# Performance work log

Hardware: AMD Instinct MI355X
Metric: run time of the kernel (lower is better)

The kernel has to match this reference:

```python
import jax, jax.numpy as jnp
import numpy as np

N = 8192
IN_DIM = 256
OUT_DIM = 256
NEG_INF = -1000000000.0
LEAKY_SLOPE = 0.2


def setup_inputs() -> dict:
    key = jax.random.key(0)
    k_h, k_adj, k_W, k_a = jax.random.split(key, 4)
    h = jax.random.normal(k_h, (N, IN_DIM), dtype=jnp.float32)
    adj = jax.random.randint(k_adj, (N, N), 0, 2, dtype=jnp.int32)
    # learned params (nn.Linear without bias stores weight [out, in]; we keep [in, out] for x @ W)
    W = jax.random.normal(k_W, (IN_DIM, OUT_DIM), dtype=jnp.float32) / np.sqrt(IN_DIM)
    a = jax.random.normal(k_a, (OUT_DIM,), dtype=jnp.float32) / np.sqrt(OUT_DIM)
    return {"h": h, "adj": adj, "W": W, "a": a}


def reference(h, adj, W, a):
    Wh = h @ W                                   # [N, out_dim]
    f = Wh @ a                                   # [N]
    e = jax.nn.leaky_relu(f[:, None] + f[None, :], LEAKY_SLOPE)  # [N, N]
    mask = (adj > 0).astype(Wh.dtype)
    e_masked = e * mask + (1.0 - mask) * NEG_INF
    alpha = jax.nn.softmax(e_masked, axis=1)     # [N, N]
    h_prime = alpha @ Wh                         # [N, out_dim]
    return jax.nn.elu(h_prime), alpha
```

## Files before the change

kernel.cpp:

```cpp
#include <hip/hip_runtime.h>
#include <hip/hip_bf16.h>

#define NROW 8192
#define DIM 256

typedef short bf16x8 __attribute__((ext_vector_type(8)));
typedef float f32x4 __attribute__((ext_vector_type(4)));

__device__ __forceinline__ short f2bf(float x) {
    return __builtin_bit_cast(short, __float2bfloat16(x));
}

__device__ __forceinline__ void gload_lds16(const void* g, void* l) {
    __builtin_amdgcn_global_load_lds(
        (const __attribute__((address_space(1))) unsigned int*)g,
        (__attribute__((address_space(3))) unsigned int*)l, 16, 0, 0);
}

__global__ __launch_bounds__(256) void k1_whgemm(
    const float* __restrict__ h, const float* __restrict__ W,
    const float* __restrict__ a, short* __restrict__ whbT,
    float* __restrict__ f)
{
    __shared__ float hs[64][65];
    __shared__ float wsm[64][65];
    const int tid = threadIdx.x;
    const int tx = tid & 15, ty = tid >> 4;
    const int i0 = blockIdx.x * 64;
    const int n0 = blockIdx.y * 64;

    float acc[4][4];
#pragma unroll
    for (int u = 0; u < 4; ++u)
#pragma unroll
        for (int v = 0; v < 4; ++v) acc[u][v] = 0.f;

    for (int kb = 0; kb < DIM; kb += 64) {
#pragma unroll
        for (int rr = 0; rr < 4; ++rr) {
            int row = rr * 16 + ty;
            *(float4*)&hs[row][tx * 4] =
                *(const float4*)&h[(size_t)(i0 + row) * DIM + kb + tx * 4];
            *(float4*)&wsm[row][tx * 4] =
                *(const float4*)&W[(size_t)(kb + row) * DIM + n0 + tx * 4];
        }
        __syncthreads();
#pragma unroll 8
        for (int kk = 0; kk < 64; ++kk) {
            float av[4], bv[4];
#pragma unroll
            for (int u = 0; u < 4; ++u) av[u] = hs[ty * 4 + u][kk];
#pragma unroll
            for (int v = 0; v < 4; ++v) bv[v] = wsm[kk][tx * 4 + v];
#pragma unroll
            for (int u = 0; u < 4; ++u)
#pragma unroll
                for (int v = 0; v < 4; ++v) acc[u][v] += av[u] * bv[v];
        }
        __syncthreads();
    }

#pragma unroll
    for (int u = 0; u < 4; ++u)
#pragma unroll
        for (int v = 0; v < 4; ++v) hs[ty * 4 + u][tx * 4 + v] = acc[u][v];
    __syncthreads();

    {
        int r = tid >> 2, q = tid & 3;
        float s = 0.f;
#pragma unroll
        for (int c = 0; c < 16; ++c) s += hs[r][q * 16 + c] * a[n0 + q * 16 + c];
        s += __shfl_xor(s, 1);
        s += __shfl_xor(s, 2);
        if (q == 0) atomicAdd(&f[i0 + r], s);
    }

    {
        int n = tid >> 2, q = tid & 3;
        union { short s[16]; int4 i4[2]; } pk;
#pragma unroll
        for (int b = 0; b < 4; ++b)
#pragma unroll
            for (int c = 0; c < 4; ++c)
                pk.s[b * 4 + c] = f2bf(hs[q * 16 + b * 4 + c][n]);
        size_t base = ((size_t)(i0 >> 6) * 256 + n0 + n) * 64 + q * 16;
        *(int4*)&whbT[base] = pk.i4[0];
        *(int4*)&whbT[base + 8] = pk.i4[1];
    }
}

__global__ __launch_bounds__(256) void k3d_alpha(
    const int* __restrict__ adj, const float* __restrict__ f,
    float* __restrict__ alpha)
{
    const int i = blockIdx.x;
    const int tid = threadIdx.x;
    const float fi = f[i];
    const int* row = adj + (size_t)i * NROW;

    int4 av[8];
    float4 fv[8];
#pragma unroll
    for (int it = 0; it < 8; ++it)
        av[it] = *(const int4*)&row[it * 1024 + tid * 4];
#pragma unroll
    for (int it = 0; it < 8; ++it)
        fv[it] = *(const float4*)&f[it * 1024 + tid * 4];

    float sum = 0.f;
#pragma unroll
    for (int it = 0; it < 8; ++it) {
        float x0 = fi + fv[it].x, x1 = fi + fv[it].y;
        float x2 = fi + fv[it].z, x3 = fi + fv[it].w;
        float4 t;
        t.x = av[it].x > 0 ? __expf(fmaxf(x0, 0.2f * x0)) : 0.f;
        t.y = av[it].y > 0 ? __expf(fmaxf(x1, 0.2f * x1)) : 0.f;
        t.z = av[it].z > 0 ? __expf(fmaxf(x2, 0.2f * x2)) : 0.f;
        t.w = av[it].w > 0 ? __expf(fmaxf(x3, 0.2f * x3)) : 0.f;
        fv[it] = t;
        sum += t.x + t.y + t.z + t.w;
    }

#pragma unroll
    for (int off = 32; off > 0; off >>= 1) sum += __shfl_xor(sum, off);
    __shared__ float red[4];
    if ((tid & 63) == 0) red[tid >> 6] = sum;
    __syncthreads();
    const float inv = 1.f / (red[0] + red[1] + red[2] + red[3]);

    float* arow = alpha + (size_t)i * NROW;
#pragma unroll
    for (int it = 0; it < 8; ++it) {
        float4 t = fv[it];
        float4 o = {t.x * inv, t.y * inv, t.z * inv, t.w * inv};
        *(float4*)&arow[it * 1024 + tid * 4] = o;
    }
}

__global__ __launch_bounds__(512) void k4g_gemm(
    const float* __restrict__ alpha, const short* __restrict__ whbT,
    float* __restrict__ out0)
{
    __shared__ __align__(16) short Bs[4][4096];

    const int tid = threadIdx.x;
    const int wave = tid >> 6;
    const int lane = tid & 63;
    const int lo = lane & 15;
    const int quad = lane >> 4;
    const int q8 = quad * 8;

    const int bid = blockIdx.x;
    const int xcd = bid & 7;
    const int slot = bid >> 3;
    const int rb = xcd * 8 + (slot & 7);
    const int cs = slot >> 3;
    const int i0 = rb * 128;
    const int n0 = cs * 64;

    const float* aptr = alpha + (size_t)(i0 + wave * 16 + lo) * NROW + q8;

    const int n_local = tid >> 3;
    const int schunk = ((tid & 7) ^ (n_local & 7)) * 8;

    const int bx0 = (quad ^ (lo & 7)) * 8;
    const int bx1 = ((4 + quad) ^ (lo & 7)) * 8;
    int off0[4], off1[4];
#pragma unroll
    for (int nt = 0; nt < 4; ++nt) {
        int rbase = (nt * 16 + lo) * 64;
        off0[nt] = rbase + bx0;
        off1[nt] = rbase + bx1;
    }

    f32x4 acc[4] = {};
    f32x4 aA[4], aB[4], aC[4], aD[4];

#define STAGE(buf, kt)                                                        \
    {                                                                         \
        const short* gsrc = whbT + (size_t)(kt) * 16384 +                     \
                            (n0 + n_local) * 64 + schunk;                     \
        gload_lds16(gsrc, &Bs[buf][tid * 8]);                                 \
    }

#define ALOAD(set, kt)                                                        \
    {                                                                         \
        const float* ap = aptr + (size_t)(kt) * 64;                           \
        asm volatile("global_load_dwordx4 %0, %4, off\n\t"                    \
                     "global_load_dwordx4 %1, %4, off offset:16\n\t"          \
                     "global_load_dwordx4 %2, %4, off offset:128\n\t"         \
                     "global_load_dwordx4 %3, %4, off offset:144"             \
                     : "=&v"(aA[set]), "=&v"(aB[set]),                        \
                       "=&v"(aC[set]), "=&v"(aD[set])                         \
                     : "v"(ap));                                              \
    }

#define CONSUME(c)                                                            \
    {                                                                         \
        bf16x8 af0, af1;                                                      \
        af0[0] = f2bf(aA[c][0]); af0[1] = f2bf(aA[c][1]);                     \
        af0[2] = f2bf(aA[c][2]); af0[3] = f2bf(aA[c][3]);                     \
        af0[4] = f2bf(aB[c][0]); af0[5] = f2bf(aB[c][1]);                     \
        af0[6] = f2bf(aB[c][2]); af0[7] = f2bf(aB[c][3]);                     \
        af1[0] = f2bf(aC[c][0]); af1[1] = f2bf(aC[c][1]);                     \
        af1[2] = f2bf(aC[c][2]); af1[3] = f2bf(aC[c][3]);                     \
        af1[4] = f2bf(aD[c][0]); af1[5] = f2bf(aD[c][1]);                     \
        af1[6] = f2bf(aD[c][2]); af1[7] = f2bf(aD[c][3]);                     \
        _Pragma("unroll")                                                     \
        for (int nt = 0; nt < 4; ++nt) {                                      \
            bf16x8 b0 = *(const bf16x8*)&Bs[c][off0[nt]];                     \
            acc[nt] = __builtin_amdgcn_mfma_f32_16x16x32_bf16(af0, b0,        \
                                                          acc[nt], 0, 0, 0);  \
            bf16x8 b1 = *(const bf16x8*)&Bs[c][off1[nt]];                     \
            acc[nt] = __builtin_amdgcn_mfma_f32_16x16x32_bf16(af1, b1,        \
                                                          acc[nt], 0, 0, 0);  \
        }                                                                     \
    }

#define KSTEP(kt, c, DO, N)                                                   \
    {                                                                         \
        if (DO) { STAGE(((c) + 2) & 3, (kt) + 2); ALOAD(((c) + 2) & 3,        \
                                                        (kt) + 2); }          \
        asm volatile("s_waitcnt vmcnt(" #N ")" ::: "memory");                 \
        __builtin_amdgcn_s_barrier();                                         \
        __builtin_amdgcn_sched_barrier(0);                                    \
        CONSUME(c)                                                            \
    }

    STAGE(0, 0); ALOAD(0, 0);
    STAGE(1, 1); ALOAD(1, 1);

#pragma unroll 1
    for (int base = 0; base < 124; base += 4) {
        KSTEP(base + 0, 0, true, 10)
        KSTEP(base + 1, 1, true, 10)
        KSTEP(base + 2, 2, true, 10)
        KSTEP(base + 3, 3, true, 10)
    }
    KSTEP(124, 0, true, 10)
    KSTEP(125, 1, true, 10)
    KSTEP(126, 2, false, 5)
    KSTEP(127, 3, false, 0)

#undef STAGE
#undef ALOAD
#undef CONSUME
#undef KSTEP

    const int ccb = n0 + lo;
#pragma unroll
    for (int nt = 0; nt < 4; ++nt) {
#pragma unroll
        for (int c = 0; c < 4; ++c) {
            const int rr = i0 + wave * 16 + quad * 4 + c;
            float v = acc[nt][c];
            v = v > 0.f ? v : __expf(v) - 1.f;
            out0[(size_t)rr * DIM + ccb + nt * 16] = v;
        }
    }
}

extern "C" void kernel_launch(void* const* d_in, const int* in_sizes, int n_in,
                              void* d_out, int out_size, void* d_ws, size_t ws_size,
                              hipStream_t stream) {
    const float* h = (const float*)d_in[0];
    const int* adj = (const int*)d_in[1];
    const float* W = (const float*)d_in[2];
    const float* a = (const float*)d_in[3];
    float* out0 = (float*)d_out;
    float* alpha = out0 + (size_t)NROW * DIM;

    char* ws = (char*)d_ws;
    float* f = (float*)ws;
    short* whbT = (short*)(ws + 32768);

    hipMemsetAsync(f, 0, NROW * sizeof(float), stream);
    k1_whgemm<<<dim3(NROW / 64, DIM / 64), 256, 0, stream>>>(h, W, a, whbT, f);
    k3d_alpha<<<dim3(NROW), 256, 0, stream>>>(adj, f, alpha);
    k4g_gemm<<<dim3(256), 512, 0, stream>>>(alpha, whbT, out0);
}
```

Baseline: 607.7 us.

## Fuse softmax alpha computation into the alpha@Wh GEMM kernel

Merges the separate alpha kernel into the GEMM kernel. Each GEMM block first streams its 128 rows of adj to compute the softmax row sums, then recomputes the exp values from adj on the fly during the MFMA loop. Each of the 4 column-slice blocks writes a quarter of alpha to the output. This removes the GEMM's reread of the fp32 alpha matrix and one launch, at the cost of reading adj twice per column slice (8 times in total) and redundant exp work across the 4 column blocks.

```diff
diff --git a/kernel.cpp b/kernel.cpp
--- a/kernel.cpp
+++ b/kernel.cpp
@@ -15,6 +15,28 @@
     __builtin_amdgcn_global_load_lds(
         (const __attribute__((address_space(1))) unsigned int*)g,
         (__attribute__((address_space(3))) unsigned int*)l, 16, 0, 0);
+}
+
+__device__ __forceinline__ float lrexpi(int m, float fj, float fi) {
+    float x = fi + fj;
+    return m > 0 ? __expf(fmaxf(x, 0.2f * x)) : 0.f;
+}
+__device__ __forceinline__ float sum4i(int4 m, float4 fv, float fi) {
+    return lrexpi(m.x, fv.x, fi) + lrexpi(m.y, fv.y, fi) +
+           lrexpi(m.z, fv.z, fi) + lrexpi(m.w, fv.w, fi);
+}
+__device__ __forceinline__ float lrexpb(float bits, float fj, float fi) {
+    int m = __builtin_bit_cast(int, bits);
+    float x = fi + fj;
+    return m > 0 ? __expf(fmaxf(x, 0.2f * x)) : 0.f;
+}
+__device__ __forceinline__ float4 lrexp4(f32x4 a, float4 fv, float fi) {
+    float4 r;
+    r.x = lrexpb(a[0], fv.x, fi);
+    r.y = lrexpb(a[1], fv.y, fi);
+    r.z = lrexpb(a[2], fv.z, fi);
+    r.w = lrexpb(a[3], fv.w, fi);
+    return r;
 }
 
 __global__ __launch_bounds__(256) void k1_whgemm(
@@ -90,58 +112,12 @@
     }
 }
 
-__global__ __launch_bounds__(256) void k3d_alpha(
+__global__ __launch_bounds__(512) void k45_fused(
     const int* __restrict__ adj, const float* __restrict__ f,
-    float* __restrict__ alpha)
-{
-    const int i = blockIdx.x;
-    const int tid = threadIdx.x;
-    const float fi = f[i];
-    const int* row = adj + (size_t)i * NROW;
-
-    int4 av[8];
-    float4 fv[8];
-#pragma unroll
-    for (int it = 0; it < 8; ++it)
-        av[it] = *(const int4*)&row[it * 1024 + tid * 4];
-#pragma unroll
-    for (int it = 0; it < 8; ++it)
-        fv[it] = *(const float4*)&f[it * 1024 + tid * 4];
-
-    float sum = 0.f;
-#pragma unroll
-    for (int it = 0; it < 8; ++it) {
-        float x0 = fi + fv[it].x, x1 = fi + fv[it].y;
-        float x2 = fi + fv[it].z, x3 = fi + fv[it].w;
-        float4 t;
-        t.x = av[it].x > 0 ? __expf(fmaxf(x0, 0.2f * x0)) : 0.f;
-        t.y = av[it].y > 0 ? __expf(fmaxf(x1, 0.2f * x1)) : 0.f;
-        t.z = av[it].z > 0 ? __expf(fmaxf(x2, 0.2f * x2)) : 0.f;
-        t.w = av[it].w > 0 ? __expf(fmaxf(x3, 0.2f * x3)) : 0.f;
-        fv[it] = t;
-        sum += t.x + t.y + t.z + t.w;
-    }
-
-#pragma unroll
-    for (int off = 32; off > 0; off >>= 1) sum += __shfl_xor(sum, off);
-    __shared__ float red[4];
-    if ((tid & 63) == 0) red[tid >> 6] = sum;
-    __syncthreads();
-    const float inv = 1.f / (red[0] + red[1] + red[2] + red[3]);
-
-    float* arow = alpha + (size_t)i * NROW;
-#pragma unroll
-    for (int it = 0; it < 8; ++it) {
-        float4 t = fv[it];
-        float4 o = {t.x * inv, t.y * inv, t.z * inv, t.w * inv};
-        *(float4*)&arow[it * 1024 + tid * 4] = o;
-    }
-}
-
-__global__ __launch_bounds__(512) void k4g_gemm(
-    const float* __restrict__ alpha, const short* __restrict__ whbT,
+    const short* __restrict__ whbT, float* __restrict__ alpha,
     float* __restrict__ out0)
 {
+    __shared__ float f_sh[NROW];
     __shared__ __align__(16) short Bs[4][4096];
 
     const int tid = threadIdx.x;
@@ -159,11 +135,59 @@
     const int i0 = rb * 128;
     const int n0 = cs * 64;
 
-    const float* aptr = alpha + (size_t)(i0 + wave * 16 + lo) * NROW + q8;
+#pragma unroll
+    for (int u = 0; u < 4; ++u)
+        *(float4*)&f_sh[u * 2048 + tid * 4] =
+            *(const float4*)&f[u * 2048 + tid * 4];
+    __syncthreads();
+
+    const int myrow = i0 + wave * 16 + lo;
+    const float fi = f_sh[myrow];
+    const int* adji = adj + (size_t)myrow * NROW + q8;
+
+    float rsum = 0.f;
+    {
+        int4 A0, A1, A2, A3, B0, B1, B2, B3;
+        int4 C0, C1, C2, C3, D0, D1, D2, D3;
+
+#define LOADI(P, kt)                                                          \
+        {                                                                     \
+            const int* p = adji + (size_t)(kt) * 64;                          \
+            P##0 = *(const int4*)p;                                           \
+            P##1 = *(const int4*)(p + 4);                                     \
+            P##2 = *(const int4*)(p + 32);                                    \
+            P##3 = *(const int4*)(p + 36);                                    \
+        }
+
+#define SUMI(P, kt)                                                           \
+        {                                                                     \
+            float4 F0 = *(const float4*)&f_sh[(kt) * 64 + q8];                \
+            float4 F1 = *(const float4*)&f_sh[(kt) * 64 + q8 + 4];            \
+            float4 F2 = *(const float4*)&f_sh[(kt) * 64 + 32 + q8];           \
+            float4 F3 = *(const float4*)&f_sh[(kt) * 64 + 36 + q8];           \
+            rsum += sum4i(P##0, F0, fi) + sum4i(P##1, F1, fi) +               \
+                    sum4i(P##2, F2, fi) + sum4i(P##3, F3, fi);                \
+        }
+
+        LOADI(A, 0) LOADI(B, 1) LOADI(C, 2) LOADI(D, 3)
+#pragma unroll 1
+        for (int kt = 0; kt < 124; kt += 4) {
+            SUMI(A, kt)     LOADI(A, kt + 4)
+            SUMI(B, kt + 1) LOADI(B, kt + 5)
+            SUMI(C, kt + 2) LOADI(C, kt + 6)
+            SUMI(D, kt + 3) LOADI(D, kt + 7)
+        }
+        SUMI(A, 124) SUMI(B, 125) SUMI(C, 126) SUMI(D, 127)
+#undef LOADI
+#undef SUMI
+    }
+
+    rsum += __shfl_xor(rsum, 16);
+    rsum += __shfl_xor(rsum, 32);
+    const float inv = 1.f / rsum;
 
     const int n_local = tid >> 3;
     const int schunk = ((tid & 7) ^ (n_local & 7)) * 8;
-
     const int bx0 = (quad ^ (lo & 7)) * 8;
     const int bx1 = ((4 + quad) ^ (lo & 7)) * 8;
     int off0[4], off1[4];
@@ -174,8 +198,10 @@
         off1[nt] = rbase + bx1;
     }
 
+    const float* adjp = (const float*)adji;
+
+    f32x4 pA[4], pB[4], pC[4], pD[4];
     f32x4 acc[4] = {};
-    f32x4 aA[4], aB[4], aC[4], aD[4];
 
 #define STAGE(buf, kt)                                                        \
     {                                                                         \
@@ -186,27 +212,50 @@
 
 #define ALOAD(set, kt)                                                        \
     {                                                                         \
-        const float* ap = aptr + (size_t)(kt) * 64;                           \
+        const float* ap = adjp + (size_t)(kt) * 64;                           \
         asm volatile("global_load_dwordx4 %0, %4, off\n\t"                    \
                      "global_load_dwordx4 %1, %4, off offset:16\n\t"          \
                      "global_load_dwordx4 %2, %4, off offset:128\n\t"         \
                      "global_load_dwordx4 %3, %4, off offset:144"             \
-                     : "=&v"(aA[set]), "=&v"(aB[set]),                        \
-                       "=&v"(aC[set]), "=&v"(aD[set])                         \
+                     : "=&v"(pA[set]), "=&v"(pB[set]),                        \
+                       "=&v"(pC[set]), "=&v"(pD[set])                         \
                      : "v"(ap));                                              \
     }
 
-#define CONSUME(c)                                                            \
+#define CONSUME(c, kt)                                                        \
     {                                                                         \
+        float4 F0 = *(const float4*)&f_sh[(kt) * 64 + q8];                    \
+        float4 F1 = *(const float4*)&f_sh[(kt) * 64 + q8 + 4];                \
+        float4 F2 = *(const float4*)&f_sh[(kt) * 64 + 32 + q8];               \
+        float4 F3 = *(const float4*)&f_sh[(kt) * 64 + 36 + q8];               \
+        float4 t0 = lrexp4(pA[c], F0, fi);                                    \
+        float4 t1 = lrexp4(pB[c], F1, fi);                                    \
+        float4 t2 = lrexp4(pC[c], F2, fi);                                    \
+        float4 t3 = lrexp4(pD[c], F3, fi);                                    \
+        float4 s0 = make_float4(t0.x * inv, t0.y * inv, t0.z * inv,           \
+                                t0.w * inv);                                  \
+        float4 s1 = make_float4(t1.x * inv, t1.y * inv, t1.z * inv,           \
+                                t1.w * inv);                                  \
+        float4 s2 = make_float4(t2.x * inv, t2.y * inv, t2.z * inv,           \
+                                t2.w * inv);                                  \
+        float4 s3 = make_float4(t3.x * inv, t3.y * inv, t3.z * inv,           \
+                                t3.w * inv);                                  \
+        if (((kt) & 3) == cs) {                                               \
+            float* arow = alpha + (size_t)myrow * NROW + (kt) * 64 + q8;      \
+            *(float4*)arow = s0;                                              \
+            *(float4*)(arow + 4) = s1;                                        \
+            *(float4*)(arow + 32) = s2;                                       \
+            *(float4*)(arow + 36) = s3;                                       \
+        }                                                                     \
         bf16x8 af0, af1;                                                      \
-        af0[0] = f2bf(aA[c][0]); af0[1] = f2bf(aA[c][1]);                     \
-        af0[2] = f2bf(aA[c][2]); af0[3] = f2bf(aA[c][3]);                     \
-        af0[4] = f2bf(aB[c][0]); af0[5] = f2bf(aB[c][1]);                     \
-        af0[6] = f2bf(aB[c][2]); af0[7] = f2bf(aB[c][3]);                     \
-        af1[0] = f2bf(aC[c][0]); af1[1] = f2bf(aC[c][1]);                     \
-        af1[2] = f2bf(aC[c][2]); af1[3] = f2bf(aC[c][3]);                     \
-        af1[4] = f2bf(aD[c][0]); af1[5] = f2bf(aD[c][1]);                     \
-        af1[6] = f2bf(aD[c][2]); af1[7] = f2bf(aD[c][3]);                     \
+        af0[0] = f2bf(s0.x); af0[1] = f2bf(s0.y);                             \
+        af0[2] = f2bf(s0.z); af0[3] = f2bf(s0.w);                             \
+        af0[4] = f2bf(s1.x); af0[5] = f2bf(s1.y);                             \
+        af0[6] = f2bf(s1.z); af0[7] = f2bf(s1.w);                             \
+        af1[0] = f2bf(s2.x); af1[1] = f2bf(s2.y);                             \
+        af1[2] = f2bf(s2.z); af1[3] = f2bf(s2.w);                             \
+        af1[4] = f2bf(s3.x); af1[5] = f2bf(s3.y);                             \
+        af1[6] = f2bf(s3.z); af1[7] = f2bf(s3.w);                             \
         _Pragma("unroll")                                                     \
         for (int nt = 0; nt < 4; ++nt) {                                      \
             bf16x8 b0 = *(const bf16x8*)&Bs[c][off0[nt]];                     \
@@ -225,7 +274,7 @@
         asm volatile("s_waitcnt vmcnt(" #N ")" ::: "memory");                 \
         __builtin_amdgcn_s_barrier();                                         \
         __builtin_amdgcn_sched_barrier(0);                                    \
-        CONSUME(c)                                                            \
+        CONSUME(c, kt)                                                        \
     }
 
     STAGE(0, 0); ALOAD(0, 0);
@@ -277,6 +326,5 @@
 
     hipMemsetAsync(f, 0, NROW * sizeof(float), stream);
     k1_whgemm<<<dim3(NROW / 64, DIM / 64), 256, 0, stream>>>(h, W, a, whbT, f);
-    k3d_alpha<<<dim3(NROW), 256, 0, stream>>>(adj, f, alpha);
-    k4g_gemm<<<dim3(256), 512, 0, stream>>>(alpha, whbT, out0);
-}
+    k45_fused<<<dim3(256), 512, 0, stream>>>(adj, f, whbT, alpha, out0);
+}
```

New measurement: 720.6 us. 18.6% more time.
